# Kernel optimization log

Hardware: AMD Instinct MI355X
Metric: run time of the kernel (lower is better)

The kernel has to match this reference:

```python
import jax, jax.numpy as jnp
import numpy as np
import math

DIM = 96; HEADS = 3; WS = 4; SS = 2; RES = 48; B = 2
N = WS ** 3  # tokens per window
LOG2_8 = math.log2(8.0)


def _rel_coords_table():
    c = np.arange(-(WS - 1), WS, dtype=np.float32)
    t = np.stack(np.meshgrid(c, c, c, indexing='ij'), axis=-1)
    t = t / (WS - 1)
    t = t * 8.0
    t = np.sign(t) * np.log2(np.abs(t) + 1.0) / LOG2_8
    return t.reshape(-1, 3)


def _rel_pos_index():
    coords = np.stack(np.meshgrid(np.arange(WS), np.arange(WS), np.arange(WS), indexing='ij'))
    cf = coords.reshape(3, -1)
    rel = (cf[:, :, None] - cf[:, None, :]).transpose(1, 2, 0).copy()
    rel[:, :, 0] += WS - 1; rel[:, :, 1] += WS - 1; rel[:, :, 2] += WS - 1
    rel[:, :, 0] *= (2 * WS - 1) * (2 * WS - 1)
    rel[:, :, 1] *= (2 * WS - 1)
    return rel.sum(-1).reshape(-1)  # (N*N,)


def _attn_mask():
    H = W = D = RES
    img = np.zeros((H, W, D), np.float32)
    cnt = 0
    sl = (slice(0, -WS), slice(-WS, -SS), slice(-SS, None))
    for h in sl:
        for w in sl:
            for d in sl:
                img[h, w, d] = cnt
                cnt += 1
    m = img.reshape(H // WS, WS, W // WS, WS, D // WS, WS)
    m = m.transpose(0, 2, 4, 1, 3, 5).reshape(-1, N)
    am = m[:, None, :] - m[:, :, None]
    return np.where(am != 0, np.float32(-100.0), np.float32(0.0))  # (nW, N, N)


def _win_part(x):
    Bx, H, W, D, C = x.shape
    x = x.reshape(Bx, H // WS, WS, W // WS, WS, D // WS, WS, C)
    x = x.transpose(0, 1, 3, 5, 2, 4, 6, 7)
    return x.reshape(-1, N, C)


def _win_rev(w, Bx, H, W, D):
    C = w.shape[-1]
    x = w.reshape(Bx, H // WS, W // WS, D // WS, WS, WS, WS, C)
    x = x.transpose(0, 1, 4, 2, 5, 3, 6, 7)
    return x.reshape(Bx, H, W, D, C)


def _ln(x, g, b, eps=1e-5):
    mu = jnp.mean(x, axis=-1, keepdims=True)
    var = jnp.mean(jnp.square(x - mu), axis=-1, keepdims=True)
    return (x - mu) * jax.lax.rsqrt(var + eps) * g + b


def setup_inputs() -> dict:
    key = jax.random.key(0)
    ks = jax.random.split(key, 8)
    s = 0.02
    return {
        'x': jax.random.normal(ks[0], (B, RES, RES, RES, DIM), jnp.float32),
        'qkv_w': jax.random.normal(ks[1], (3 * DIM, DIM), jnp.float32) * s,
        'q_bias': jnp.zeros((DIM,), jnp.float32),
        'v_bias': jnp.zeros((DIM,), jnp.float32),
        'logit_scale': jnp.full((HEADS, 1, 1), math.log(10.0), jnp.float32),
        'cpb_w1': jax.random.normal(ks[2], (512, 3), jnp.float32) * s,
        'cpb_b1': jnp.zeros((512,), jnp.float32),
        'cpb_w2': jax.random.normal(ks[3], (HEADS, 512), jnp.float32) * s,
        'proj_w': jax.random.normal(ks[4], (DIM, DIM), jnp.float32) * s,
        'proj_b': jnp.zeros((DIM,), jnp.float32),
        'norm1_g': jnp.ones((DIM,), jnp.float32),
        'norm1_b': jnp.zeros((DIM,), jnp.float32),
        'fc1_w': jax.random.normal(ks[5], (4 * DIM, DIM), jnp.float32) * s,
        'fc1_b': jnp.zeros((4 * DIM,), jnp.float32),
        'fc2_w': jax.random.normal(ks[6], (DIM, 4 * DIM), jnp.float32) * s,
        'fc2_b': jnp.zeros((DIM,), jnp.float32),
        'norm2_g': jnp.ones((DIM,), jnp.float32),
        'norm2_b': jnp.zeros((DIM,), jnp.float32),
    }


def reference(x, qkv_w, q_bias, v_bias, logit_scale, cpb_w1, cpb_b1, cpb_w2,
              proj_w, proj_b, norm1_g, norm1_b, fc1_w, fc1_b, fc2_w, fc2_b,
              norm2_g, norm2_b):
    Bx, H, W, D, C = x.shape
    hd = C // HEADS
    rct = jnp.asarray(_rel_coords_table())
    rpi = _rel_pos_index()
    amask = jnp.asarray(_attn_mask())  # (nW, N, N)

    # cyclic shift + window partition
    shifted = jnp.roll(x, (-SS, -SS, -SS), axis=(1, 2, 3))
    xw = _win_part(shifted)  # (B*nW, N, C)
    B_ = xw.shape[0]; nW = B_ // Bx

    # qkv (k has no bias in SwinV2)
    bias = jnp.concatenate([q_bias, jnp.zeros_like(q_bias), v_bias])
    qkv = (xw @ qkv_w.T + bias).reshape(B_, N, 3, HEADS, hd).transpose(2, 0, 3, 1, 4)
    q, k, v = qkv[0], qkv[1], qkv[2]

    # cosine attention with clamped learnable logit scale
    qn = q / jnp.maximum(jnp.linalg.norm(q, axis=-1, keepdims=True), 1e-12)
    kn = k / jnp.maximum(jnp.linalg.norm(k, axis=-1, keepdims=True), 1e-12)
    attn = jnp.einsum('bhnd,bhmd->bhnm', qn, kn)
    scale = jnp.exp(jnp.minimum(logit_scale, math.log(1.0 / 0.01)))  # (HEADS,1,1)
    attn = attn * scale[None]

    # continuous relative position bias via small MLP + lookup
    tbl = jax.nn.relu(rct @ cpb_w1.T + cpb_b1) @ cpb_w2.T  # (T, HEADS)
    rpb = tbl[rpi].reshape(N, N, HEADS).transpose(2, 0, 1)
    rpb = 16.0 * jax.nn.sigmoid(rpb)
    attn = attn + rpb[None]

    # shift-window mask + softmax
    attn = attn.reshape(Bx, nW, HEADS, N, N) + amask[None, :, None]
    attn = jax.nn.softmax(attn.reshape(B_, HEADS, N, N), axis=-1)

    out = jnp.einsum('bhnm,bhmd->bnhd', attn, v).reshape(B_, N, C)
    out = out @ proj_w.T + proj_b

    # reverse windows + reverse shift
    aw = _win_rev(out.reshape(B_, WS, WS, WS, C), Bx, H, W, D)
    aw = jnp.roll(aw, (SS, SS, SS), axis=(1, 2, 3))

    # SwinV2 post-norm residuals
    x = x + _ln(aw, norm1_g, norm1_b)
    h = jax.nn.gelu(x @ fc1_w.T + fc1_b, approximate=False) @ fc2_w.T + fc2_b
    x = x + _ln(h, norm2_g, norm2_b)
    return x
```

## Files before the change

kernel.cpp:

```cpp
#include <hip/hip_runtime.h>
#include <math.h>

#define RES   48
#define WS    4
#define SSH   2
#define DIM   96
#define HEADS 3
#define HD    32
#define NTOK  64
#define NWAX  12
#define NWIN  (NWAX*NWAX*NWAX)

#define TSTR 104
#define VSTR 72
#define PSTR 72
#define HSTR 200

typedef float f32x4 __attribute__((ext_vector_type(4)));
typedef short s16x8 __attribute__((ext_vector_type(8)));

__device__ __forceinline__ short f2bf(float f) {
    unsigned u = __builtin_bit_cast(unsigned, f);
    u = (u + 0x7FFFu + ((u >> 16) & 1u)) >> 16;
    return (short)u;
}
__device__ __forceinline__ float bf2f(short s) {
    unsigned u = ((unsigned)(unsigned short)s) << 16;
    return __builtin_bit_cast(float, u);
}
__device__ __forceinline__ unsigned cvt_pk(float lo, float hi) {
    unsigned r;
    asm("v_cvt_pk_bf16_f32 %0, %1, %2" : "=v"(r) : "v"(lo), "v"(hi));
    return r;
}
__device__ __forceinline__ float gelu_f(float a) {
    float z = a*(1.5957691216057308f + 0.07135481627159927f*a*a);
    return a / (1.0f + __expf(-z));
}
__device__ __forceinline__ int region(int g) {
    return (g < RES - WS) ? 0 : ((g < RES - SSH) ? 1 : 2);
}
__device__ __forceinline__ int tok_xbase(int b, int wh, int ww, int wd, int t) {
    int gh = wh*WS + (t >> 4);
    int gw = ww*WS + ((t >> 2) & 3);
    int gd = wd*WS + (t & 3);
    int sh = gh + SSH; if (sh >= RES) sh -= RES;
    int sw = gw + SSH; if (sw >= RES) sw -= RES;
    int sd = gd + SSH; if (sd >= RES) sd -= RES;
    return (((b*RES + sh)*RES + sw)*RES + sd)*DIM;
}
__device__ __forceinline__ int tok_cnt(int wh, int ww, int wd, int t) {
    return region(wh*WS + (t >> 4))*9 + region(ww*WS + ((t >> 2) & 3))*3
         + region(wd*WS + (t & 3));
}

__global__ void prep_kernel(const float* __restrict__ cw1, const float* __restrict__ cb1,
                            const float* __restrict__ cw2,
                            const float* __restrict__ fc1_w, const float* __restrict__ fc2_w,
                            const float* __restrict__ qkv_w, const float* __restrict__ proj_w,
                            float* __restrict__ tbl,
                            short* __restrict__ w1p, short* __restrict__ w2p,
                            short* __restrict__ qkvp, short* __restrict__ projp) {
    int bid = blockIdx.x;
    if (bid < 343) {
        __shared__ float hid[512];
        int ti = bid;
        int a = ti / 49, b = (ti / 7) % 7, c = ti % 7;
        float comp[3] = {(float)(a - 3), (float)(b - 3), (float)(c - 3)};
        float f[3];
        #pragma unroll
        for (int k = 0; k < 3; ++k) {
            float u = (comp[k] / 3.0f) * 8.0f;
            float s = (u > 0.f) ? 1.f : ((u < 0.f) ? -1.f : 0.f);
            f[k] = s * log2f(fabsf(u) + 1.0f) * (1.0f / 3.0f);
        }
        for (int j = threadIdx.x; j < 512; j += blockDim.x) {
            float acc = cb1[j] + f[0]*cw1[j*3+0] + f[1]*cw1[j*3+1] + f[2]*cw1[j*3+2];
            hid[j] = fmaxf(acc, 0.f);
        }
        __syncthreads();
        int tid = threadIdx.x;
        if (tid < 192) {
            int h = tid >> 6, lane = tid & 63;
            float p = 0.f;
            for (int j = lane; j < 512; j += 64) p += cw2[h*512 + j] * hid[j];
            #pragma unroll
            for (int off = 32; off; off >>= 1) p += __shfl_down(p, off, 64);
            if (lane == 0) tbl[ti*3 + h] = p;
        }
    } else if (bid < 343 + 144) {
        int i = (bid - 343)*256 + threadIdx.x;
        if (i >= 36864) return;
        {
            int o = i / 96, c = i - o*96;
            int H = o / 192, rem = o - H*192;
            int wv = rem / 48, n3 = (rem - wv*48) >> 4;
            int tile = ((H*12 + wv*3 + n3)*3) + (c >> 5);
            int lane = ((c >> 3) & 3)*16 + (o & 15);
            w1p[tile*512 + lane*8 + (c & 7)] = f2bf(fc1_w[i]);
        }
        {
            int co = i / 384, oo = i - co*384;
            int tile = (co >> 4)*12 + (oo >> 5);
            int lane = ((oo >> 3) & 3)*16 + (co & 15);
            w2p[tile*512 + lane*8 + (oo & 7)] = f2bf(fc2_w[i]);
        }
    } else {
        int i = (bid - 487)*256 + threadIdx.x;
        if (i < 288*96) {
            int o = i / 96, c = i - o*96;
            int tile = (o >> 4)*3 + (c >> 5);
            int lane = ((c >> 3) & 3)*16 + (o & 15);
            qkvp[tile*512 + lane*8 + (c & 7)] = f2bf(qkv_w[i]);
        }
        if (i < 96*96) {
            int co = i / 96, k = i - co*96;
            int tile = (co >> 4)*3 + (k >> 5);
            int lane = ((k >> 3) & 3)*16 + (co & 15);
            projp[tile*512 + lane*8 + (k & 7)] = f2bf(proj_w[i]);
        }
    }
}

__global__ void rpb_kernel(const float* __restrict__ tbl, float* __restrict__ rpb) {
    int bi = blockIdx.x;
    int h = bi >> 6, i = bi & 63;
    int j = threadIdx.x;
    int hi = i >> 4, wi = (i >> 2) & 3, di = i & 3;
    int hj = j >> 4, wj = (j >> 2) & 3, dj = j & 3;
    int idx = (hi - hj + 3)*49 + (wi - wj + 3)*7 + (di - dj + 3);
    float v = tbl[idx*3 + h];
    rpb[(h*64 + i)*64 + j] = 16.0f / (1.0f + expf(-v));
}

__global__ __launch_bounds__(256, 3)
void swin_fused_kernel(const float* __restrict__ x, const short* __restrict__ qkvp,
                       const float* __restrict__ q_bias, const float* __restrict__ v_bias,
                       const float* __restrict__ logit_scale,
                       const short* __restrict__ projp, const float* __restrict__ proj_b,
                       const float* __restrict__ rpb,
                       const float* __restrict__ g1, const float* __restrict__ b1v,
                       const short* __restrict__ w1p, const float* __restrict__ fc1_b,
                       const short* __restrict__ w2p, const float* __restrict__ fc2_b,
                       const float* __restrict__ g2, const float* __restrict__ b2v,
                       float* __restrict__ out) {
    __shared__ __align__(16) char pool[41984];
    short* x_s = (short*)(pool);
    short* k_s = (short*)(pool + 13312);
    short* vT  = (short*)(pool + 26624);
    float* qn_t = (float*)(pool + 40448);
    float* kn_t = qn_t + 192;
    short* q_s  = x_s;
    short* p_s  = k_s;
    short* ao_s = x_s;
    short* x1b  = x_s;
    short* hb   = (short*)(pool + 13312);

    int tid = threadIdx.x;
    int l   = tid & 63;
    int w   = __builtin_amdgcn_readfirstlane(tid >> 6);
    int lc  = l & 15;
    int lg  = l >> 4;

    int wid = blockIdx.x;
    int b   = wid / NWIN;
    int rem = wid - b*NWIN;
    int wh = rem / (NWAX*NWAX);
    int ww = (rem / NWAX) % NWAX;
    int wd = rem % NWAX;

    for (int idx = tid; idx < NTOK*12; idx += 256) {
        int r = idx / 12, g = idx - r*12;
        const float* src = x + tok_xbase(b, wh, ww, wd, r) + g*8;
        float4 a = *reinterpret_cast<const float4*>(src);
        float4 c = *reinterpret_cast<const float4*>(src + 4);
        uint4 v;
        v.x = cvt_pk(a.x, a.y); v.y = cvt_pk(a.z, a.w);
        v.z = cvt_pk(c.x, c.y); v.w = cvt_pk(c.z, c.w);
        *reinterpret_cast<uint4*>(&x_s[r*TSTR + g*8]) = v;
    }
    __syncthreads();

    s16x8 af[3][4];
    #pragma unroll
    for (int ks = 0; ks < 3; ++ks)
        #pragma unroll
        for (int tt = 0; tt < 4; ++tt)
            af[ks][tt] = *reinterpret_cast<const s16x8*>(&x_s[(tt*16+lc)*TSTR + ks*32 + lg*8]);
    __syncthreads();

    for (int nt = w; nt < 18; nt += 4) {
        int od0 = nt*16 + lg*4;
        f32x4 C[4];
        if (nt < 6) {
            float4 qb = *reinterpret_cast<const float4*>(&q_bias[od0]);
            #pragma unroll
            for (int tt = 0; tt < 4; ++tt) C[tt] = f32x4{qb.x, qb.y, qb.z, qb.w};
        } else if (nt >= 12) {
            float4 vb = *reinterpret_cast<const float4*>(&v_bias[od0 - 192]);
            #pragma unroll
            for (int tt = 0; tt < 4; ++tt) C[tt] = f32x4{vb.x, vb.y, vb.z, vb.w};
        } else {
            #pragma unroll
            for (int tt = 0; tt < 4; ++tt) C[tt] = f32x4{0.f, 0.f, 0.f, 0.f};
        }
        #pragma unroll
        for (int ks = 0; ks < 3; ++ks) {
            s16x8 wf = *reinterpret_cast<const s16x8*>(&qkvp[(nt*3+ks)*512 + l*8]);
            #pragma unroll
            for (int tt = 0; tt < 4; ++tt)
                C[tt] = __builtin_amdgcn_mfma_f32_16x16x32_bf16(wf, af[ks][tt], C[tt], 0, 0, 0);
        }
        if (nt < 6) {
            #pragma unroll
            for (int tt = 0; tt < 4; ++tt) {
                uint2 pv;
                pv.x = cvt_pk(C[tt][0], C[tt][1]);
                pv.y = cvt_pk(C[tt][2], C[tt][3]);
                *reinterpret_cast<uint2*>(&q_s[(tt*16+lc)*TSTR + nt*16 + lg*4]) = pv;
            }
        } else if (nt < 12) {
            #pragma unroll
            for (int tt = 0; tt < 4; ++tt) {
                uint2 pv;
                pv.x = cvt_pk(C[tt][0], C[tt][1]);
                pv.y = cvt_pk(C[tt][2], C[tt][3]);
                *reinterpret_cast<uint2*>(&k_s[(tt*16+lc)*TSTR + (nt-6)*16 + lg*4]) = pv;
            }
        } else {
            int vd0 = (nt-12)*16 + lg*4;
            #pragma unroll
            for (int tt = 0; tt < 4; ++tt) {
                unsigned pA = cvt_pk(C[tt][0], C[tt][1]);
                unsigned pB = cvt_pk(C[tt][2], C[tt][3]);
                int tok = tt*16 + lc;
                vT[(vd0+0)*VSTR + tok] = (short)pA;
                vT[(vd0+1)*VSTR + tok] = (short)(pA >> 16);
                vT[(vd0+2)*VSTR + tok] = (short)pB;
                vT[(vd0+3)*VSTR + tok] = (short)(pB >> 16);
            }
        }
    }

    int cq = tok_cnt(wh, ww, wd, w*16 + lc);
    float biasv[3][4][4];
    {
        int ck[4][4];
        #pragma unroll
        for (int nt = 0; nt < 4; ++nt)
            #pragma unroll
            for (int r = 0; r < 4; ++r)
                ck[nt][r] = tok_cnt(wh, ww, wd, nt*16 + lg*4 + r);
        #pragma unroll
        for (int h = 0; h < 3; ++h)
            #pragma unroll
            for (int nt = 0; nt < 4; ++nt) {
                float4 bv = *reinterpret_cast<const float4*>(
                    &rpb[(h*64 + w*16 + lc)*64 + nt*16 + lg*4]);
                biasv[h][nt][0] = (cq != ck[nt][0]) ? bv.x - 100.0f : bv.x;
                biasv[h][nt][1] = (cq != ck[nt][1]) ? bv.y - 100.0f : bv.y;
                biasv[h][nt][2] = (cq != ck[nt][2]) ? bv.z - 100.0f : bv.z;
                biasv[h][nt][3] = (cq != ck[nt][3]) ? bv.w - 100.0f : bv.w;
            }
    }
    __syncthreads();

    if (w < 3) {
        int h = w, i = l;
        float kn = 0.f, qn = 0.f;
        #pragma unroll
        for (int c = 0; c < 4; ++c) {
            s16x8 kv = *reinterpret_cast<const s16x8*>(&k_s[i*TSTR + h*32 + c*8]);
            s16x8 qv = *reinterpret_cast<const s16x8*>(&q_s[i*TSTR + h*32 + c*8]);
            #pragma unroll
            for (int e = 0; e < 8; ++e) {
                float fk = bf2f(kv[e]); kn += fk*fk;
                float fq = bf2f(qv[e]); qn += fq*fq;
            }
        }
        float sc = __expf(fminf(logit_scale[h], 4.605170185988092f));
        kn_t[h*64 + i] = 1.0f / fmaxf(sqrtf(kn), 1e-12f);
        qn_t[h*64 + i] = sc / fmaxf(sqrtf(qn), 1e-12f);
    }

    f32x4 sc_[3][4];
    {
        s16x8 aq[3];
        #pragma unroll
        for (int h = 0; h < 3; ++h)
            aq[h] = *reinterpret_cast<const s16x8*>(&q_s[(w*16+lc)*TSTR + h*32 + lg*8]);
        #pragma unroll
        for (int h = 0; h < 3; ++h)
            #pragma unroll
            for (int nt = 0; nt < 4; ++nt) {
                s16x8 bk = *reinterpret_cast<const s16x8*>(&k_s[(nt*16+lc)*TSTR + h*32 + lg*8]);
                sc_[h][nt] = __builtin_amdgcn_mfma_f32_16x16x32_bf16(bk, aq[h], f32x4{0.f,0.f,0.f,0.f}, 0, 0, 0);
            }
    }
    __syncthreads();

    #pragma unroll
    for (int h = 0; h < 3; ++h) {
        float qnf = qn_t[h*64 + w*16 + lc];
        #pragma unroll
        for (int nt = 0; nt < 4; ++nt) {
            float4 kn4 = *reinterpret_cast<const float4*>(&kn_t[h*64 + nt*16 + lg*4]);
            sc_[h][nt][0] = sc_[h][nt][0]*qnf*kn4.x + biasv[h][nt][0];
            sc_[h][nt][1] = sc_[h][nt][1]*qnf*kn4.y + biasv[h][nt][1];
            sc_[h][nt][2] = sc_[h][nt][2]*qnf*kn4.z + biasv[h][nt][2];
            sc_[h][nt][3] = sc_[h][nt][3]*qnf*kn4.w + biasv[h][nt][3];
        }
        float mm = -1e30f;
        #pragma unroll
        for (int nt = 0; nt < 4; ++nt)
            #pragma unroll
            for (int r = 0; r < 4; ++r) mm = fmaxf(mm, sc_[h][nt][r]);
        mm = fmaxf(mm, __shfl_xor(mm, 16, 64));
        mm = fmaxf(mm, __shfl_xor(mm, 32, 64));
        float ll = 0.f;
        #pragma unroll
        for (int nt = 0; nt < 4; ++nt)
            #pragma unroll
            for (int r = 0; r < 4; ++r) {
                float ee = __expf(sc_[h][nt][r] - mm);
                sc_[h][nt][r] = ee;
                ll += ee;
            }
        ll += __shfl_xor(ll, 16, 64);
        ll += __shfl_xor(ll, 32, 64);
        float linv = 1.0f / ll;

        #pragma unroll
        for (int nt = 0; nt < 4; ++nt) {
            uint2 pv;
            pv.x = cvt_pk(sc_[h][nt][0], sc_[h][nt][1]);
            pv.y = cvt_pk(sc_[h][nt][2], sc_[h][nt][3]);
            *reinterpret_cast<uint2*>(&p_s[(w*16+lc)*PSTR + nt*16 + lg*4]) = pv;
        }

        s16x8 ap[2];
        #pragma unroll
        for (int ks = 0; ks < 2; ++ks)
            ap[ks] = *reinterpret_cast<const s16x8*>(&p_s[(w*16+lc)*PSTR + ks*32 + lg*8]);
        #pragma unroll
        for (int dt = 0; dt < 2; ++dt) {
            f32x4 o = {0.f, 0.f, 0.f, 0.f};
            #pragma unroll
            for (int ks = 0; ks < 2; ++ks) {
                s16x8 av = *reinterpret_cast<const s16x8*>(&vT[(h*32 + dt*16 + lc)*VSTR + ks*32 + lg*8]);
                o = __builtin_amdgcn_mfma_f32_16x16x32_bf16(av, ap[ks], o, 0, 0, 0);
            }
            uint2 pv;
            pv.x = cvt_pk(o[0]*linv, o[1]*linv);
            pv.y = cvt_pk(o[2]*linv, o[3]*linv);
            *reinterpret_cast<uint2*>(&ao_s[(w*16+lc)*TSTR + h*32 + dt*16 + lg*4]) = pv;
        }
    }

    float yv[6][4];
    {
        s16x8 aa[3];
        #pragma unroll
        for (int ks = 0; ks < 3; ++ks)
            aa[ks] = *reinterpret_cast<const s16x8*>(&ao_s[(w*16+lc)*TSTR + ks*32 + lg*8]);
        #pragma unroll
        for (int nt = 0; nt < 6; ++nt) {
            float bias = proj_b[nt*16 + lc];
            f32x4 C = f32x4{bias, bias, bias, bias};
            #pragma unroll
            for (int ks = 0; ks < 3; ++ks) {
                s16x8 bf = *reinterpret_cast<const s16x8*>(&projp[(nt*3+ks)*512 + l*8]);
                C = __builtin_amdgcn_mfma_f32_16x16x32_bf16(aa[ks], bf, C, 0, 0, 0);
            }
            #pragma unroll
            for (int r = 0; r < 4; ++r) yv[nt][r] = C[r];
        }
    }

    #pragma unroll
    for (int r = 0; r < 4; ++r) {
        float s = 0.f, sq = 0.f;
        #pragma unroll
        for (int n = 0; n < 6; ++n) { float v = yv[n][r]; s += v; sq += v*v; }
        #pragma unroll
        for (int m = 1; m < 16; m <<= 1) { s += __shfl_xor(s, m, 64); sq += __shfl_xor(sq, m, 64); }
        float mu  = s * (1.0f/DIM);
        float var = sq * (1.0f/DIM) - mu*mu;
        float rs  = rsqrtf(fmaxf(var, 0.f) + 1e-5f);
        int t = w*16 + lg*4 + r;
        int xb = tok_xbase(b, wh, ww, wd, t);
        #pragma unroll
        for (int n2 = 0; n2 < 3; ++n2) {
            int c0 = n2*32 + lc;
            float v0 = x[xb + c0]      + (yv[n2*2][r]   - mu)*rs*g1[c0]    + b1v[c0];
            float v1 = x[xb + c0 + 16] + (yv[n2*2+1][r] - mu)*rs*g1[c0+16] + b1v[c0+16];
            unsigned pk = cvt_pk(v0, v1);
            x1b[t*TSTR + c0]      = (short)pk;
            x1b[t*TSTR + c0 + 16] = (short)(pk >> 16);
        }
    }
    __syncthreads();

    s16x8 afx[3];
    #pragma unroll
    for (int ks = 0; ks < 3; ++ks)
        afx[ks] = *reinterpret_cast<const s16x8*>(&x1b[(w*16 + lc)*TSTR + ks*32 + lg*8]);

    f32x4 acc2[6];
    #pragma unroll
    for (int n = 0; n < 6; ++n) {
        float bb = fc2_b[n*16 + lc];
        acc2[n] = f32x4{bb, bb, bb, bb};
    }
    #pragma unroll
    for (int H = 0; H < 2; ++H) {
        f32x4 acc1[12];
        #pragma unroll
        for (int j = 0; j < 12; ++j) {
            float bb = fc1_b[H*192 + j*16 + lc];
            acc1[j] = f32x4{bb, bb, bb, bb};
        }
        #pragma unroll
        for (int ks = 0; ks < 3; ++ks)
            #pragma unroll
            for (int j = 0; j < 12; ++j) {
                s16x8 bf = *reinterpret_cast<const s16x8*>(&w1p[((H*12 + j)*3 + ks)*512 + l*8]);
                acc1[j] = __builtin_amdgcn_mfma_f32_16x16x32_bf16(afx[ks], bf, acc1[j], 0, 0, 0);
            }
        #pragma unroll
        for (int j = 0; j < 12; ++j) {
            int col = j*16 + lc;
            unsigned pA = cvt_pk(gelu_f(acc1[j][0]), gelu_f(acc1[j][1]));
            unsigned pB = cvt_pk(gelu_f(acc1[j][2]), gelu_f(acc1[j][3]));
            int row = w*16 + lg*4;
            hb[(row+0)*HSTR + col] = (short)pA;
            hb[(row+1)*HSTR + col] = (short)(pA >> 16);
            hb[(row+2)*HSTR + col] = (short)pB;
            hb[(row+3)*HSTR + col] = (short)(pB >> 16);
        }
        #pragma unroll
        for (int ksp = 0; ksp < 6; ++ksp) {
            s16x8 afh = *reinterpret_cast<const s16x8*>(&hb[(w*16 + lc)*HSTR + ksp*32 + lg*8]);
            #pragma unroll
            for (int n = 0; n < 6; ++n) {
                s16x8 bf = *reinterpret_cast<const s16x8*>(&w2p[(n*12 + H*6 + ksp)*512 + l*8]);
                acc2[n] = __builtin_amdgcn_mfma_f32_16x16x32_bf16(afh, bf, acc2[n], 0, 0, 0);
            }
        }
    }

    #pragma unroll
    for (int r = 0; r < 4; ++r) {
        float s = 0.f, sq = 0.f;
        #pragma unroll
        for (int n = 0; n < 6; ++n) { float v = acc2[n][r]; s += v; sq += v*v; }
        #pragma unroll
        for (int m = 1; m < 16; m <<= 1) { s += __shfl_xor(s, m, 64); sq += __shfl_xor(sq, m, 64); }
        float mu  = s * (1.0f/DIM);
        float var = sq * (1.0f/DIM) - mu*mu;
        float rs  = rsqrtf(fmaxf(var, 0.f) + 1e-5f);
        int t = w*16 + lg*4 + r;
        int xb = tok_xbase(b, wh, ww, wd, t);
        #pragma unroll
        for (int n = 0; n < 6; ++n) {
            int c = n*16 + lc;
            float x1f = bf2f(x1b[t*TSTR + c]);
            out[xb + c] = x1f + (acc2[n][r] - mu)*rs*g2[c] + b2v[c];
        }
    }
}

extern "C" void kernel_launch(void* const* d_in, const int* in_sizes, int n_in,
                              void* d_out, int out_size, void* d_ws, size_t ws_size,
                              hipStream_t stream) {
    const float* x      = (const float*)d_in[0];
    const float* qkv_w  = (const float*)d_in[1];
    const float* q_bias = (const float*)d_in[2];
    const float* v_bias = (const float*)d_in[3];
    const float* lscale = (const float*)d_in[4];
    const float* cpb_w1 = (const float*)d_in[5];
    const float* cpb_b1 = (const float*)d_in[6];
    const float* cpb_w2 = (const float*)d_in[7];
    const float* proj_w = (const float*)d_in[8];
    const float* proj_b = (const float*)d_in[9];
    const float* n1g    = (const float*)d_in[10];
    const float* n1b    = (const float*)d_in[11];
    const float* fc1_w  = (const float*)d_in[12];
    const float* fc1_b  = (const float*)d_in[13];
    const float* fc2_w  = (const float*)d_in[14];
    const float* fc2_b  = (const float*)d_in[15];
    const float* n2g    = (const float*)d_in[16];
    const float* n2b    = (const float*)d_in[17];
    float* out = (float*)d_out;

    char* wsb = (char*)d_ws;
    float* tbl  = (float*)wsb;
    float* rpb  = (float*)(wsb + 8192);
    short* w1p  = (short*)(wsb + 65536);
    short* w2p  = (short*)(wsb + 65536 + 73728);
    short* qkvp = (short*)(wsb + 65536 + 147456);
    short* projp= qkvp + 27648;

    prep_kernel<<<595, 256, 0, stream>>>(cpb_w1, cpb_b1, cpb_w2, fc1_w, fc2_w,
                                         qkv_w, proj_w, tbl, w1p, w2p, qkvp, projp);
    rpb_kernel<<<192, 64, 0, stream>>>(tbl, rpb);
    swin_fused_kernel<<<2*NWIN, 256, 0, stream>>>(x, qkvp, q_bias, v_bias, lscale,
                                                  projp, proj_b, rpb,
                                                  n1g, n1b, w1p, fc1_b, w2p, fc2_b,
                                                  n2g, n2b, out);
}
```

Measured before the change: 169.7 us.

## Fuse rpb table into prep kernel, cache token bases, drop softmax max

Merges the CPB MLP and the rpb expansion into the prep kernel, so each of the 12288 bias entries recomputes its 512-wide MLP directly and one launch is removed. The fused window kernel now precomputes per-token global offsets and region counts into shared memory instead of recomputing them repeatedly. Softmax drops the max-subtraction pass, relying on the cosine-attention logits being bounded; this risks overflow only if logit_scale were large. The per-element MLP in prep does redundant work (512 iterations per thread) that may lengthen the prep stage.

```diff
diff --git a/kernel.cpp b/kernel.cpp
--- a/kernel.cpp
+++ b/kernel.cpp
@@ -58,38 +58,12 @@
                             const float* __restrict__ cw2,
                             const float* __restrict__ fc1_w, const float* __restrict__ fc2_w,
                             const float* __restrict__ qkv_w, const float* __restrict__ proj_w,
-                            float* __restrict__ tbl,
+                            float* __restrict__ rpb,
                             short* __restrict__ w1p, short* __restrict__ w2p,
                             short* __restrict__ qkvp, short* __restrict__ projp) {
     int bid = blockIdx.x;
-    if (bid < 343) {
-        __shared__ float hid[512];
-        int ti = bid;
-        int a = ti / 49, b = (ti / 7) % 7, c = ti % 7;
-        float comp[3] = {(float)(a - 3), (float)(b - 3), (float)(c - 3)};
-        float f[3];
-        #pragma unroll
-        for (int k = 0; k < 3; ++k) {
-            float u = (comp[k] / 3.0f) * 8.0f;
-            float s = (u > 0.f) ? 1.f : ((u < 0.f) ? -1.f : 0.f);
-            f[k] = s * log2f(fabsf(u) + 1.0f) * (1.0f / 3.0f);
-        }
-        for (int j = threadIdx.x; j < 512; j += blockDim.x) {
-            float acc = cb1[j] + f[0]*cw1[j*3+0] + f[1]*cw1[j*3+1] + f[2]*cw1[j*3+2];
-            hid[j] = fmaxf(acc, 0.f);
-        }
-        __syncthreads();
-        int tid = threadIdx.x;
-        if (tid < 192) {
-            int h = tid >> 6, lane = tid & 63;
-            float p = 0.f;
-            for (int j = lane; j < 512; j += 64) p += cw2[h*512 + j] * hid[j];
-            #pragma unroll
-            for (int off = 32; off; off >>= 1) p += __shfl_down(p, off, 64);
-            if (lane == 0) tbl[ti*3 + h] = p;
-        }
-    } else if (bid < 343 + 144) {
-        int i = (bid - 343)*256 + threadIdx.x;
+    if (bid < 144) {
+        int i = bid*256 + threadIdx.x;
         if (i >= 36864) return;
         {
             int o = i / 96, c = i - o*96;
@@ -105,8 +79,8 @@
             int lane = ((oo >> 3) & 3)*16 + (co & 15);
             w2p[tile*512 + lane*8 + (oo & 7)] = f2bf(fc2_w[i]);
         }
-    } else {
-        int i = (bid - 487)*256 + threadIdx.x;
+    } else if (bid < 252) {
+        int i = (bid - 144)*256 + threadIdx.x;
         if (i < 288*96) {
             int o = i / 96, c = i - o*96;
             int tile = (o >> 4)*3 + (c >> 5);
@@ -119,18 +93,31 @@
             int lane = ((k >> 3) & 3)*16 + (co & 15);
             projp[tile*512 + lane*8 + (k & 7)] = f2bf(proj_w[i]);
         }
-    }
-}
-
-__global__ void rpb_kernel(const float* __restrict__ tbl, float* __restrict__ rpb) {
-    int bi = blockIdx.x;
-    int h = bi >> 6, i = bi & 63;
-    int j = threadIdx.x;
-    int hi = i >> 4, wi = (i >> 2) & 3, di = i & 3;
-    int hj = j >> 4, wj = (j >> 2) & 3, dj = j & 3;
-    int idx = (hi - hj + 3)*49 + (wi - wj + 3)*7 + (di - dj + 3);
-    float v = tbl[idx*3 + h];
-    rpb[(h*64 + i)*64 + j] = 16.0f / (1.0f + expf(-v));
+    } else {
+        int flat = (bid - 252)*256 + threadIdx.x;
+        int h = flat >> 12;
+        int rem = flat & 4095;
+        int i = rem >> 6, j = rem & 63;
+        int hi = i >> 4, wi = (i >> 2) & 3, di = i & 3;
+        int hj = j >> 4, wj = (j >> 2) & 3, dj = j & 3;
+        int idx = (hi - hj + 3)*49 + (wi - wj + 3)*7 + (di - dj + 3);
+        int a = idx / 49, bq = (idx / 7) % 7, cq = idx % 7;
+        float comp[3] = {(float)(a - 3), (float)(bq - 3), (float)(cq - 3)};
+        float f[3];
+        #pragma unroll
+        for (int k = 0; k < 3; ++k) {
+            float u = (comp[k] / 3.0f) * 8.0f;
+            float s = (u > 0.f) ? 1.f : ((u < 0.f) ? -1.f : 0.f);
+            f[k] = s * log2f(fabsf(u) + 1.0f) * (1.0f / 3.0f);
+        }
+        float p = 0.f;
+        #pragma unroll 4
+        for (int jj = 0; jj < 512; ++jj) {
+            float acc = cb1[jj] + f[0]*cw1[jj*3+0] + f[1]*cw1[jj*3+1] + f[2]*cw1[jj*3+2];
+            p += cw2[h*512 + jj] * fmaxf(acc, 0.f);
+        }
+        rpb[(h*64 + i)*64 + j] = 16.0f / (1.0f + expf(-p));
+    }
 }
 
 __global__ __launch_bounds__(256, 3)
@@ -144,12 +131,14 @@
                        const short* __restrict__ w2p, const float* __restrict__ fc2_b,
                        const float* __restrict__ g2, const float* __restrict__ b2v,
                        float* __restrict__ out) {
-    __shared__ __align__(16) char pool[41984];
+    __shared__ __align__(16) char pool[42496];
     short* x_s = (short*)(pool);
     short* k_s = (short*)(pool + 13312);
     short* vT  = (short*)(pool + 26624);
     float* qn_t = (float*)(pool + 40448);
     float* kn_t = qn_t + 192;
+    int* xbase_s = (int*)(pool + 41984);
+    int* cnt_s   = (int*)(pool + 42240);
     short* q_s  = x_s;
     short* p_s  = k_s;
     short* ao_s = x_s;
@@ -169,9 +158,15 @@
     int ww = (rem / NWAX) % NWAX;
     int wd = rem % NWAX;
 
+    if (tid < NTOK) {
+        xbase_s[tid] = tok_xbase(b, wh, ww, wd, tid);
+        cnt_s[tid]   = tok_cnt(wh, ww, wd, tid);
+    }
+    __syncthreads();
+
     for (int idx = tid; idx < NTOK*12; idx += 256) {
         int r = idx / 12, g = idx - r*12;
-        const float* src = x + tok_xbase(b, wh, ww, wd, r) + g*8;
+        const float* src = x + xbase_s[r] + g*8;
         float4 a = *reinterpret_cast<const float4*>(src);
         float4 c = *reinterpret_cast<const float4*>(src + 4);
         uint4 v;
@@ -242,25 +237,23 @@
         }
     }
 
-    int cq = tok_cnt(wh, ww, wd, w*16 + lc);
+    int cq = cnt_s[w*16 + lc];
     float biasv[3][4][4];
     {
-        int ck[4][4];
+        int4 ck[4];
         #pragma unroll
         for (int nt = 0; nt < 4; ++nt)
-            #pragma unroll
-            for (int r = 0; r < 4; ++r)
-                ck[nt][r] = tok_cnt(wh, ww, wd, nt*16 + lg*4 + r);
+            ck[nt] = *reinterpret_cast<const int4*>(&cnt_s[nt*16 + lg*4]);
         #pragma unroll
         for (int h = 0; h < 3; ++h)
             #pragma unroll
             for (int nt = 0; nt < 4; ++nt) {
                 float4 bv = *reinterpret_cast<const float4*>(
                     &rpb[(h*64 + w*16 + lc)*64 + nt*16 + lg*4]);
-                biasv[h][nt][0] = (cq != ck[nt][0]) ? bv.x - 100.0f : bv.x;
-                biasv[h][nt][1] = (cq != ck[nt][1]) ? bv.y - 100.0f : bv.y;
-                biasv[h][nt][2] = (cq != ck[nt][2]) ? bv.z - 100.0f : bv.z;
-                biasv[h][nt][3] = (cq != ck[nt][3]) ? bv.w - 100.0f : bv.w;
+                biasv[h][nt][0] = (cq != ck[nt].x) ? bv.x - 100.0f : bv.x;
+                biasv[h][nt][1] = (cq != ck[nt].y) ? bv.y - 100.0f : bv.y;
+                biasv[h][nt][2] = (cq != ck[nt].z) ? bv.z - 100.0f : bv.z;
+                biasv[h][nt][3] = (cq != ck[nt].w) ? bv.w - 100.0f : bv.w;
             }
     }
     __syncthreads();
@@ -302,30 +295,18 @@
     #pragma unroll
     for (int h = 0; h < 3; ++h) {
         float qnf = qn_t[h*64 + w*16 + lc];
+        float ll = 0.f;
         #pragma unroll
         for (int nt = 0; nt < 4; ++nt) {
             float4 kn4 = *reinterpret_cast<const float4*>(&kn_t[h*64 + nt*16 + lg*4]);
-            sc_[h][nt][0] = sc_[h][nt][0]*qnf*kn4.x + biasv[h][nt][0];
-            sc_[h][nt][1] = sc_[h][nt][1]*qnf*kn4.y + biasv[h][nt][1];
-            sc_[h][nt][2] = sc_[h][nt][2]*qnf*kn4.z + biasv[h][nt][2];
-            sc_[h][nt][3] = sc_[h][nt][3]*qnf*kn4.w + biasv[h][nt][3];
-        }
-        float mm = -1e30f;
-        #pragma unroll
-        for (int nt = 0; nt < 4; ++nt)
-            #pragma unroll
-            for (int r = 0; r < 4; ++r) mm = fmaxf(mm, sc_[h][nt][r]);
-        mm = fmaxf(mm, __shfl_xor(mm, 16, 64));
-        mm = fmaxf(mm, __shfl_xor(mm, 32, 64));
-        float ll = 0.f;
-        #pragma unroll
-        for (int nt = 0; nt < 4; ++nt)
-            #pragma unroll
-            for (int r = 0; r < 4; ++r) {
-                float ee = __expf(sc_[h][nt][r] - mm);
-                sc_[h][nt][r] = ee;
-                ll += ee;
-            }
+            float e0 = __expf(sc_[h][nt][0]*qnf*kn4.x + biasv[h][nt][0]);
+            float e1 = __expf(sc_[h][nt][1]*qnf*kn4.y + biasv[h][nt][1]);
+            float e2 = __expf(sc_[h][nt][2]*qnf*kn4.z + biasv[h][nt][2]);
+            float e3 = __expf(sc_[h][nt][3]*qnf*kn4.w + biasv[h][nt][3]);
+            sc_[h][nt][0] = e0; sc_[h][nt][1] = e1;
+            sc_[h][nt][2] = e2; sc_[h][nt][3] = e3;
+            ll += e0 + e1 + e2 + e3;
+        }
         ll += __shfl_xor(ll, 16, 64);
         ll += __shfl_xor(ll, 32, 64);
         float linv = 1.0f / ll;
@@ -377,6 +358,9 @@
         }
     }
 
+    int xbr[4];
+    #pragma unroll
+    for (int r = 0; r < 4; ++r) xbr[r] = xbase_s[w*16 + lg*4 + r];
     #pragma unroll
     for (int r = 0; r < 4; ++r) {
         float s = 0.f, sq = 0.f;
@@ -388,7 +372,7 @@
         float var = sq * (1.0f/DIM) - mu*mu;
         float rs  = rsqrtf(fmaxf(var, 0.f) + 1e-5f);
         int t = w*16 + lg*4 + r;
-        int xb = tok_xbase(b, wh, ww, wd, t);
+        int xb = xbr[r];
         #pragma unroll
         for (int n2 = 0; n2 < 3; ++n2) {
             int c0 = n2*32 + lc;
@@ -460,7 +444,7 @@
         float var = sq * (1.0f/DIM) - mu*mu;
         float rs  = rsqrtf(fmaxf(var, 0.f) + 1e-5f);
         int t = w*16 + lg*4 + r;
-        int xb = tok_xbase(b, wh, ww, wd, t);
+        int xb = xbr[r];
         #pragma unroll
         for (int n = 0; n < 6; ++n) {
             int c = n*16 + lc;
@@ -494,16 +478,14 @@
     float* out = (float*)d_out;
 
     char* wsb = (char*)d_ws;
-    float* tbl  = (float*)wsb;
     float* rpb  = (float*)(wsb + 8192);
     short* w1p  = (short*)(wsb + 65536);
     short* w2p  = (short*)(wsb + 65536 + 73728);
     short* qkvp = (short*)(wsb + 65536 + 147456);
     short* projp= qkvp + 27648;
 
-    prep_kernel<<<595, 256, 0, stream>>>(cpb_w1, cpb_b1, cpb_w2, fc1_w, fc2_w,
-                                         qkv_w, proj_w, tbl, w1p, w2p, qkvp, projp);
-    rpb_kernel<<<192, 64, 0, stream>>>(tbl, rpb);
+    prep_kernel<<<300, 256, 0, stream>>>(cpb_w1, cpb_b1, cpb_w2, fc1_w, fc2_w,
+                                         qkv_w, proj_w, rpb, w1p, w2p, qkvp, projp);
     swin_fused_kernel<<<2*NWIN, 256, 0, stream>>>(x, qkvp, q_bias, v_bias, lscale,
                                                   projp, proj_b, rpb,
                                                   n1g, n1b, w1p, fc1_b, w2p, fc2_b,
```

After: 208.2 us. 22.7% more time.
